# Optimization experiments

Measured on AMD Instinct MI355X. Metric: run time of the kernel, lower is better.

## Reference

```python
import jax, jax.numpy as jnp
import numpy as np

EPS = 1e-12  # torch F.normalize eps


def setup_inputs() -> dict:
    key = jax.random.key(0)
    k1, k2, k3 = jax.random.split(key, 3)
    B, D, H, W, K = 64, 512, 32, 32, 64
    x = jax.random.normal(k1, (B, D, H, W), dtype=jnp.float32)
    w = jax.random.normal(k2, (K, D), dtype=jnp.float32) * 0.05  # 1x1 conv weight
    c = jax.random.normal(k3, (K, D), dtype=jnp.float32)          # cluster centers
    return {"x": x, "w": w, "c": c}


def reference(x, w, c):
    B, D, H, W = x.shape
    K = w.shape[0]
    N = H * W
    # 1x1 conv (no bias): (B,D,H,W) x (K,D) -> (B,K,H,W)
    features = jnp.einsum('bdhw,kd->bkhw', x, w)
    # NOTE: original applies softmax over dim=2 (the H axis only)
    a_bar = jax.nn.softmax(features, axis=2)
    xf = x.reshape(B, D, N)
    a = a_bar.reshape(B, K, N)
    # V[b,k,d] = sum_n a[b,k,n] * (x[b,d,n] - c[k,d])
    V = jnp.einsum('bkn,bdn->bkd', a, xf) - a.sum(axis=2)[:, :, None] * c[None]
    V = V.transpose(2, 1, 0)  # (D, K, B)
    # F.normalize(V, p=2, dim=1) applied twice (second is idempotent)
    norm = jnp.maximum(jnp.linalg.norm(V, axis=1, keepdims=True), EPS)
    y = V / norm
    norm2 = jnp.maximum(jnp.linalg.norm(y, axis=1, keepdims=True), EPS)
    return y / norm2
```

## Files before the change

kernel.cpp:

```cpp
#include <hip/hip_runtime.h>


typedef __attribute__((ext_vector_type(8))) short short8;
typedef __attribute__((ext_vector_type(4))) float f32x4;
typedef unsigned short u16;
typedef unsigned int u32;

union S8u { u32 q[4]; short8 s; };

__device__ __forceinline__ u32 pk2(float lo, float hi) {
  union { float f; u32 u; } a, b; a.f = lo; b.f = hi;
  u32 xl = (a.u + 0x7fffu + ((a.u >> 16) & 1u)) >> 16;
  u32 xh = (b.u + 0x7fffu + ((b.u >> 16) & 1u)) & 0xffff0000u;
  return xl | xh;
}

__device__ __forceinline__ u16 bf1(float f) {
  union { float f; u32 u; } a; a.f = f;
  return (u16)((a.u + 0x7fffu + ((a.u >> 16) & 1u)) >> 16);
}

typedef const __attribute__((address_space(1))) u32 GU32;
typedef __attribute__((address_space(3))) u32 LU32;
__device__ __forceinline__ void glds16(const void* g, void* l) {
  __builtin_amdgcn_global_load_lds((GU32*)g, (LU32*)l, 16, 0, 0);
}

__global__ __launch_bounds__(256, 2) void k1_features(
    const float* __restrict__ x, const float* __restrict__ wgt,
    float* __restrict__ feat)
{
  const int blk = blockIdx.x;
  const int b = blk & 63, nt8 = blk >> 6;
  const int nb = nt8 * 128;
  const int tid = threadIdx.x, lane = tid & 63, wv = tid >> 6;
  const int row = lane & 15, q = lane >> 4;

  __shared__ __align__(16) float xs[2][32][128];

  const char* xbase = (const char*)(x + ((size_t)b << 19) + nb);
  const int dd0 = tid >> 5, cby = (tid & 31) * 16;
  const float* wrow = wgt + row * 512 + q * 8;

  f32x4 acc[4][2];
#pragma unroll
  for (int mt = 0; mt < 4; mt++)
#pragma unroll
    for (int nt = 0; nt < 2; nt++) acc[mt][nt] = (f32x4){0.f, 0.f, 0.f, 0.f};

#define STAGE1(d0, buf)                                                        \
  {                                                                            \
    char* lx = (char*)&xs[buf][0][0];                                          \
    _Pragma("unroll")                                                          \
    for (int j = 0; j < 4; j++)                                                \
      glds16(xbase + (size_t)((d0) + j * 8 + dd0) * 4096 + cby,                \
             lx + j * 4096 + tid * 16);                                        \
  }

  STAGE1(0, 0);
  f32x4 wa[4][2];
#pragma unroll
  for (int mt = 0; mt < 4; mt++) {
    wa[mt][0] = *(const f32x4*)(wrow + mt * 8192);
    wa[mt][1] = *(const f32x4*)(wrow + mt * 8192 + 4);
  }

  for (int i = 0; i < 16; i++) {
    const int buf = i & 1;
    __syncthreads();
    short8 af[4];
#pragma unroll
    for (int mt = 0; mt < 4; mt++) {
      S8u t;
      t.q[0] = pk2(wa[mt][0][0], wa[mt][0][1]); t.q[1] = pk2(wa[mt][0][2], wa[mt][0][3]);
      t.q[2] = pk2(wa[mt][1][0], wa[mt][1][1]); t.q[3] = pk2(wa[mt][1][2], wa[mt][1][3]);
      af[mt] = t.s;
    }
    if (i < 15) {
      STAGE1((i + 1) * 32, buf ^ 1);
      const float* wn = wrow + (i + 1) * 32;
#pragma unroll
      for (int mt = 0; mt < 4; mt++) {
        wa[mt][0] = *(const f32x4*)(wn + mt * 8192);
        wa[mt][1] = *(const f32x4*)(wn + mt * 8192 + 4);
      }
    }
    short8 bfv[2];
#pragma unroll
    for (int nt = 0; nt < 2; nt++) {
      const int n = wv * 32 + nt * 16 + row;
      const int d8 = q * 8;
      float v0 = xs[buf][d8 + 0][n], v1 = xs[buf][d8 + 1][n];
      float v2 = xs[buf][d8 + 2][n], v3 = xs[buf][d8 + 3][n];
      float v4 = xs[buf][d8 + 4][n], v5 = xs[buf][d8 + 5][n];
      float v6 = xs[buf][d8 + 6][n], v7 = xs[buf][d8 + 7][n];
      S8u t;
      t.q[0] = pk2(v0, v1); t.q[1] = pk2(v2, v3);
      t.q[2] = pk2(v4, v5); t.q[3] = pk2(v6, v7);
      bfv[nt] = t.s;
    }
#pragma unroll
    for (int nt = 0; nt < 2; nt++)
#pragma unroll
      for (int mt = 0; mt < 4; mt++)
        acc[mt][nt] = __builtin_amdgcn_mfma_f32_16x16x32_bf16(af[mt], bfv[nt], acc[mt][nt], 0, 0, 0);
  }
#undef STAGE1

  float* fb = feat + ((size_t)b << 16);
  const int nbw = nb + wv * 32;
#pragma unroll
  for (int mt = 0; mt < 4; mt++)
#pragma unroll
    for (int nt = 0; nt < 2; nt++)
#pragma unroll
      for (int r = 0; r < 4; r++)
        fb[(mt * 16 + q * 4 + r) * 1024 + nbw + nt * 16 + row] = acc[mt][nt][r];
}

__global__ __launch_bounds__(256) void k1b_softmax(
    const float* __restrict__ feat, u16* __restrict__ am)
{
  const int tid = threadIdx.x, lane = tid & 63, wv = tid >> 6;
  const int rid = blockIdx.x * 4 + wv;
  const float* f = feat + ((size_t)rid << 10);
  u16* ar = am + ((size_t)rid << 10);
  const int w = lane & 31, half = lane >> 5;
  const int base = w + half * 512;
  float v[16];
  float m = -1e30f;
#pragma unroll
  for (int i = 0; i < 16; i++) { v[i] = f[base + i * 32]; m = fmaxf(m, v[i]); }
  m = fmaxf(m, __shfl_xor(m, 32));
  float s = 0.f;
#pragma unroll
  for (int i = 0; i < 16; i++) { v[i] = __expf(v[i] - m); s += v[i]; }
  s += __shfl_xor(s, 32);
  const float inv = 1.0f / s;
#pragma unroll
  for (int i = 0; i < 16; i++) ar[base + i * 32] = bf1(v[i] * inv);
}

__global__ __launch_bounds__(256, 2) void k2_aggregate(
    const float* __restrict__ x, const u16* __restrict__ am,
    const float* __restrict__ cc, float* __restrict__ yw)
{
  const int blk = blockIdx.x;
  const int b = blk & 63, dt = blk >> 6;
  const int tid = threadIdx.x, lane = tid & 63, wv = tid >> 6;
  const int row = lane & 15, q = lane >> 4;

  __shared__ __align__(16) float xs[2][2048];

  const char* xbase = (const char*)(x + ((size_t)b << 19) + (size_t)dt * 64 * 1024);
  const u16* ab = am + ((size_t)b << 16) + row * 1024 + q * 8;
  const int r0 = tid >> 3, s0g = tid & 7;

#define STAGE2(n0, buf)                                                        \
  {                                                                            \
    char* lxs = (char*)&xs[buf][0];                                            \
    _Pragma("unroll")                                                          \
    for (int j = 0; j < 2; j++) {                                              \
      const int r = j * 32 + r0;                                               \
      const int col = ((s0g * 4) + ((r & 3) << 3)) & 31;                       \
      glds16(xbase + (size_t)r * 4096 + (size_t)((n0) + col) * 4,              \
             lxs + (j * 256 + tid) * 16);                                      \
    }                                                                          \
  }

  f32x4 acc[4];
#pragma unroll
  for (int mt = 0; mt < 4; mt++) acc[mt] = (f32x4){0.f, 0.f, 0.f, 0.f};

  STAGE2(0, 0);
  short8 sa[4];
#pragma unroll
  for (int mt = 0; mt < 4; mt++) sa[mt] = *(const short8*)(ab + mt * 16384);

  const int rB = wv * 16 + row;
  const int slot = (2 * q - 2 * (rB & 3)) & 7;
  const int fidx = rB * 32 + slot * 4;

  for (int i = 0; i < 32; i++) {
    const int buf = i & 1;
    __syncthreads();
    short8 af[4];
#pragma unroll
    for (int mt = 0; mt < 4; mt++) af[mt] = sa[mt];
    if (i < 31) {
      STAGE2((i + 1) * 32, buf ^ 1);
      const u16* an = ab + (i + 1) * 32;
#pragma unroll
      for (int mt = 0; mt < 4; mt++) sa[mt] = *(const short8*)(an + mt * 16384);
    }
    f32x4 g0 = *(const f32x4*)&xs[buf][fidx];
    f32x4 g1 = *(const f32x4*)&xs[buf][fidx + 4];
    S8u t;
    t.q[0] = pk2(g0[0], g0[1]); t.q[1] = pk2(g0[2], g0[3]);
    t.q[2] = pk2(g1[0], g1[1]); t.q[3] = pk2(g1[2], g1[3]);
    const short8 bfv = t.s;
#pragma unroll
    for (int mt = 0; mt < 4; mt++)
      acc[mt] = __builtin_amdgcn_mfma_f32_16x16x32_bf16(af[mt], bfv, acc[mt], 0, 0, 0);
  }
#undef STAGE2

  const int dcol = dt * 64 + wv * 16 + row;
  float v[16]; float ss = 0.f;
#pragma unroll
  for (int mt = 0; mt < 4; mt++)
#pragma unroll
    for (int r = 0; r < 4; r++) {
      const int k = mt * 16 + q * 4 + r;
      const float tv = acc[mt][r] - 32.0f * cc[k * 512 + dcol];
      v[mt * 4 + r] = tv; ss += tv * tv;
    }
  ss += __shfl_xor(ss, 16);
  ss += __shfl_xor(ss, 32);
  const float rn = 1.0f / fmaxf(sqrtf(ss), 1e-12f);
  float* yb = yw + ((size_t)b << 15) + dcol;
#pragma unroll
  for (int mt = 0; mt < 4; mt++)
#pragma unroll
    for (int r = 0; r < 4; r++)
      yb[(size_t)(mt * 16 + q * 4 + r) << 9] = v[mt * 4 + r] * rn;
}

__global__ __launch_bounds__(256) void k3_transpose(
    const float* __restrict__ yw, float* __restrict__ out)
{
  const int blk = blockIdx.x;
  const int k = blk & 63;
  const int dt = blk >> 6;
  const int d0 = dt * 64;
  const int tid = threadIdx.x;
  __shared__ float T[64][68];
  {
    const int bl = tid >> 2, seg = tid & 3;
    const float* src = yw + (size_t)bl * 32768 + k * 512 + d0 + seg * 16;
#pragma unroll
    for (int i = 0; i < 4; i++) {
      f32x4 v = *(const f32x4*)(src + i * 4);
#pragma unroll
      for (int jj = 0; jj < 4; jj++) T[seg * 16 + i * 4 + jj][bl] = v[jj];
    }
  }
  __syncthreads();
  {
    const int dl = tid >> 2, bseg = tid & 3;
    float* dst = out + (size_t)(d0 + dl) * 4096 + k * 64 + bseg * 16;
    const float* srcT = &T[dl][bseg * 16];
#pragma unroll
    for (int i = 0; i < 4; i++)
      *(f32x4*)(dst + i * 4) = *(const f32x4*)(srcT + i * 4);
  }
}

extern "C" void kernel_launch(void* const* d_in, const int* in_sizes, int n_in,
                              void* d_out, int out_size, void* d_ws, size_t ws_size,
                              hipStream_t stream) {
  const float* x = (const float*)d_in[0];
  const float* w = (const float*)d_in[1];
  const float* c = (const float*)d_in[2];
  float* out = (float*)d_out;
  char* ws = (char*)d_ws;
  float* feat = (float*)ws;
  u16*   a_ws = (u16*)(ws + (size_t)17 * 1024 * 1024);
  float* yw   = (float*)(ws + (size_t)26 * 1024 * 1024);
  k1_features <<<dim3(512),  dim3(256), 0, stream>>>(x, w, feat);
  k1b_softmax <<<dim3(1024), dim3(256), 0, stream>>>(feat, a_ws);
  k2_aggregate<<<dim3(512),  dim3(256), 0, stream>>>(x, a_ws, c, yw);
  k3_transpose<<<dim3(512),  dim3(256), 0, stream>>>(yw, out);
}
```

Before: 237.9 us.

## Fuse conv and H-axis softmax by tiling over W columns; reswizzle LDS

The conv kernel now tiles each block over 4 W columns across all 32 H rows, so the full softmax axis sits inside one block. The softmax is computed in shared memory and bf16 weights are written directly, which drops the fp32 feature round-trip through global memory and one kernel launch. The global-to-LDS load patterns in both the conv and aggregate kernels are reswizzled (rotation and XOR) to cut LDS bank conflicts. In exchange, global loads become 16-byte strided gathers of W quads, the softmax stores are scattered u16 writes, and the larger LDS footprint may limit occupancy.

```diff
diff --git a/kernel.cpp b/kernel.cpp
--- a/kernel.cpp
+++ b/kernel.cpp
@@ -26,20 +26,36 @@
   __builtin_amdgcn_global_load_lds((GU32*)g, (LU32*)l, 16, 0, 0);
 }
 
-__global__ __launch_bounds__(256, 2) void k1_features(
+__global__ __launch_bounds__(256, 2) void k1_conv_softmax(
     const float* __restrict__ x, const float* __restrict__ wgt,
-    float* __restrict__ feat)
+    u16* __restrict__ am)
 {
   const int blk = blockIdx.x;
-  const int b = blk & 63, nt8 = blk >> 6;
-  const int nb = nt8 * 128;
+  const int b = blk & 63, wq = blk >> 6;
+  const int w0 = wq * 4;
   const int tid = threadIdx.x, lane = tid & 63, wv = tid >> 6;
   const int row = lane & 15, q = lane >> 4;
 
-  __shared__ __align__(16) float xs[2][32][128];
-
-  const char* xbase = (const char*)(x + ((size_t)b << 19) + nb);
-  const int dd0 = tid >> 5, cby = (tid & 31) * 16;
+  __shared__ __align__(16) char smem[33792];
+  float (*F)[132] = (float (*)[132])smem;
+
+  int goff[4];
+#pragma unroll
+  for (int j2 = 0; j2 < 4; j2++) {
+    const int g = j2 * 256 + tid;
+    const int d = g >> 5, s = g & 31;
+    const int h = (s - 2 * (d >> 3)) & 31;
+    goff[j2] = d * 4096 + h * 128;
+  }
+  const char* xbase = (const char*)x + ((size_t)b << 21) + (size_t)w0 * 4;
+
+  int fbase[2];
+#pragma unroll
+  for (int nt = 0; nt < 2; nt++) {
+    const int j = wv * 32 + nt * 16 + row;
+    const int h = j >> 2, wl = j & 3;
+    fbase[nt] = q * 4096 + ((h + 2 * q) & 31) * 16 + wl * 4;
+  }
   const float* wrow = wgt + row * 512 + q * 8;
 
   f32x4 acc[4][2];
@@ -50,11 +66,11 @@
 
 #define STAGE1(d0, buf)                                                        \
   {                                                                            \
-    char* lx = (char*)&xs[buf][0][0];                                          \
+    char* lx = smem + (buf) * 16384;                                           \
     _Pragma("unroll")                                                          \
-    for (int j = 0; j < 4; j++)                                                \
-      glds16(xbase + (size_t)((d0) + j * 8 + dd0) * 4096 + cby,                \
-             lx + j * 4096 + tid * 16);                                        \
+    for (int j2 = 0; j2 < 4; j2++)                                             \
+      glds16(xbase + (size_t)(d0) * 4096 + goff[j2],                           \
+             lx + (j2 * 256 + tid) * 16);                                      \
   }
 
   STAGE1(0, 0);
@@ -88,12 +104,15 @@
     short8 bfv[2];
 #pragma unroll
     for (int nt = 0; nt < 2; nt++) {
-      const int n = wv * 32 + nt * 16 + row;
-      const int d8 = q * 8;
-      float v0 = xs[buf][d8 + 0][n], v1 = xs[buf][d8 + 1][n];
-      float v2 = xs[buf][d8 + 2][n], v3 = xs[buf][d8 + 3][n];
-      float v4 = xs[buf][d8 + 4][n], v5 = xs[buf][d8 + 5][n];
-      float v6 = xs[buf][d8 + 6][n], v7 = xs[buf][d8 + 7][n];
+      const char* p = smem + buf * 16384 + fbase[nt];
+      float v0 = *(const float*)(p);
+      float v1 = *(const float*)(p + 512);
+      float v2 = *(const float*)(p + 1024);
+      float v3 = *(const float*)(p + 1536);
+      float v4 = *(const float*)(p + 2048);
+      float v5 = *(const float*)(p + 2560);
+      float v6 = *(const float*)(p + 3072);
+      float v7 = *(const float*)(p + 3584);
       S8u t;
       t.q[0] = pk2(v0, v1); t.q[1] = pk2(v2, v3);
       t.q[2] = pk2(v4, v5); t.q[3] = pk2(v6, v7);
@@ -107,38 +126,34 @@
   }
 #undef STAGE1
 
-  float* fb = feat + ((size_t)b << 16);
-  const int nbw = nb + wv * 32;
+  __syncthreads();
 #pragma unroll
   for (int mt = 0; mt < 4; mt++)
 #pragma unroll
     for (int nt = 0; nt < 2; nt++)
 #pragma unroll
       for (int r = 0; r < 4; r++)
-        fb[(mt * 16 + q * 4 + r) * 1024 + nbw + nt * 16 + row] = acc[mt][nt][r];
-}
-
-__global__ __launch_bounds__(256) void k1b_softmax(
-    const float* __restrict__ feat, u16* __restrict__ am)
-{
-  const int tid = threadIdx.x, lane = tid & 63, wv = tid >> 6;
-  const int rid = blockIdx.x * 4 + wv;
-  const float* f = feat + ((size_t)rid << 10);
-  u16* ar = am + ((size_t)rid << 10);
-  const int w = lane & 31, half = lane >> 5;
-  const int base = w + half * 512;
-  float v[16];
-  float m = -1e30f;
-#pragma unroll
-  for (int i = 0; i < 16; i++) { v[i] = f[base + i * 32]; m = fmaxf(m, v[i]); }
-  m = fmaxf(m, __shfl_xor(m, 32));
-  float s = 0.f;
-#pragma unroll
-  for (int i = 0; i < 16; i++) { v[i] = __expf(v[i] - m); s += v[i]; }
-  s += __shfl_xor(s, 32);
-  const float inv = 1.0f / s;
-#pragma unroll
-  for (int i = 0; i < 16; i++) ar[base + i * 32] = bf1(v[i] * inv);
+        F[mt * 16 + q * 4 + r][wv * 32 + nt * 16 + row] = acc[mt][nt][r];
+  __syncthreads();
+
+  {
+    const int k = tid >> 2, wl = tid & 3;
+    float m = -1e30f;
+#pragma unroll
+    for (int h = 0; h < 32; h++) m = fmaxf(m, F[k][h * 4 + wl]);
+    float s = 0.f;
+#pragma unroll
+    for (int h = 0; h < 32; h++) {
+      const float e = __expf(F[k][h * 4 + wl] - m);
+      F[k][h * 4 + wl] = e;
+      s += e;
+    }
+    const float inv = 1.0f / s;
+    u16* ar = am + ((size_t)b << 16) + k * 1024 + w0 + wl;
+#pragma unroll
+    for (int h = 0; h < 32; h++)
+      ar[h * 32] = bf1(F[k][h * 4 + wl] * inv);
+  }
 }
 
 __global__ __launch_bounds__(256, 2) void k2_aggregate(
@@ -150,22 +165,30 @@
   const int tid = threadIdx.x, lane = tid & 63, wv = tid >> 6;
   const int row = lane & 15, q = lane >> 4;
 
-  __shared__ __align__(16) float xs[2][2048];
-
-  const char* xbase = (const char*)(x + ((size_t)b << 19) + (size_t)dt * 64 * 1024);
+  __shared__ __align__(16) char smem[16384];
+
+  int aoff[2];
+#pragma unroll
+  for (int j = 0; j < 2; j++) {
+    const int f = j * 256 + tid;
+    const int r = f >> 3, s = f & 7;
+    aoff[j] = r * 4096 + 4 * (s ^ (r & 7)) * 4;
+  }
+  const char* xbase = (const char*)x + ((size_t)b << 21) + (size_t)dt * 64 * 4096;
   const u16* ab = am + ((size_t)b << 16) + row * 1024 + q * 8;
-  const int r0 = tid >> 3, s0g = tid & 7;
+
+  const int rB = wv * 16 + row;
+  const int su = (2 * q) ^ (rB & 7);
+  const int fo0 = (rB * 8 + su) * 16;
+  const int fo1 = (rB * 8 + (su ^ 1)) * 16;
 
 #define STAGE2(n0, buf)                                                        \
   {                                                                            \
-    char* lxs = (char*)&xs[buf][0];                                            \
+    char* lx = smem + (buf) * 8192;                                            \
     _Pragma("unroll")                                                          \
-    for (int j = 0; j < 2; j++) {                                              \
-      const int r = j * 32 + r0;                                               \
-      const int col = ((s0g * 4) + ((r & 3) << 3)) & 31;                       \
-      glds16(xbase + (size_t)r * 4096 + (size_t)((n0) + col) * 4,              \
-             lxs + (j * 256 + tid) * 16);                                      \
-    }                                                                          \
+    for (int j = 0; j < 2; j++)                                                \
+      glds16(xbase + (size_t)(n0) * 4 + aoff[j],                               \
+             lx + (j * 256 + tid) * 16);                                       \
   }
 
   f32x4 acc[4];
@@ -176,10 +199,6 @@
   short8 sa[4];
 #pragma unroll
   for (int mt = 0; mt < 4; mt++) sa[mt] = *(const short8*)(ab + mt * 16384);
-
-  const int rB = wv * 16 + row;
-  const int slot = (2 * q - 2 * (rB & 3)) & 7;
-  const int fidx = rB * 32 + slot * 4;
 
   for (int i = 0; i < 32; i++) {
     const int buf = i & 1;
@@ -193,8 +212,8 @@
 #pragma unroll
       for (int mt = 0; mt < 4; mt++) sa[mt] = *(const short8*)(an + mt * 16384);
     }
-    f32x4 g0 = *(const f32x4*)&xs[buf][fidx];
-    f32x4 g1 = *(const f32x4*)&xs[buf][fidx + 4];
+    f32x4 g0 = *(const f32x4*)(smem + buf * 8192 + fo0);
+    f32x4 g1 = *(const f32x4*)(smem + buf * 8192 + fo1);
     S8u t;
     t.q[0] = pk2(g0[0], g0[1]); t.q[1] = pk2(g0[2], g0[3]);
     t.q[2] = pk2(g1[0], g1[1]); t.q[3] = pk2(g1[2], g1[3]);
@@ -264,11 +283,9 @@
   const float* c = (const float*)d_in[2];
   float* out = (float*)d_out;
   char* ws = (char*)d_ws;
-  float* feat = (float*)ws;
-  u16*   a_ws = (u16*)(ws + (size_t)17 * 1024 * 1024);
-  float* yw   = (float*)(ws + (size_t)26 * 1024 * 1024);
-  k1_features <<<dim3(512),  dim3(256), 0, stream>>>(x, w, feat);
-  k1b_softmax <<<dim3(1024), dim3(256), 0, stream>>>(feat, a_ws);
-  k2_aggregate<<<dim3(512),  dim3(256), 0, stream>>>(x, a_ws, c, yw);
-  k3_transpose<<<dim3(512),  dim3(256), 0, stream>>>(yw, out);
-}
+  u16*   a_ws = (u16*)ws;
+  float* yw   = (float*)(ws + (size_t)16 * 1024 * 1024);
+  k1_conv_softmax<<<dim3(512), dim3(256), 0, stream>>>(x, w, a_ws);
+  k2_aggregate   <<<dim3(512), dim3(256), 0, stream>>>(x, a_ws, c, yw);
+  k3_transpose   <<<dim3(512), dim3(256), 0, stream>>>(yw, out);
+}
```

Result: slower. 280.4 us (+17.9%).

## Pre-pack weights to bf16, stage via LDS, and XOR-swizzle aggregate x tiles

Applied to the files above, without the earlier changes.

Adds a small kernel that converts the 1x1 conv weights to padded bf16 tiles once per call. The features kernel then streams those tiles into LDS with async global-to-LDS loads instead of each thread loading fp32 weights and packing them every iteration. The aggregate kernel swaps its LDS staging pattern for an XOR swizzle to cut bank conflicts, and the softmax grid is remapped so blocks cover rows in batch-major order. The cost is one extra kernel launch and a little more shared memory in the features kernel.

```diff
diff --git a/kernel.cpp b/kernel.cpp
--- a/kernel.cpp
+++ b/kernel.cpp
@@ -2,6 +2,7 @@
 
 
 typedef __attribute__((ext_vector_type(8))) short short8;
+typedef __attribute__((ext_vector_type(8))) unsigned short u16x8;
 typedef __attribute__((ext_vector_type(4))) float f32x4;
 typedef unsigned short u16;
 typedef unsigned int u32;
@@ -26,8 +27,19 @@
   __builtin_amdgcn_global_load_lds((GU32*)g, (LU32*)l, 16, 0, 0);
 }
 
+__global__ __launch_bounds__(256) void k0_packw(
+    const float* __restrict__ w, u16* __restrict__ wsw)
+{
+  const int tg = blockIdx.x * 256 + threadIdx.x;
+  const int dd4 = tg & 7, i = (tg >> 3) & 15, k = tg >> 7;
+  f32x4 v = *(const f32x4*)(w + k * 512 + i * 32 + dd4 * 4);
+  u32* dst = (u32*)(wsw + ((size_t)i * 64 + k) * 40 + dd4 * 4);
+  dst[0] = pk2(v[0], v[1]);
+  dst[1] = pk2(v[2], v[3]);
+}
+
 __global__ __launch_bounds__(256, 2) void k1_features(
-    const float* __restrict__ x, const float* __restrict__ wgt,
+    const float* __restrict__ x, const u16* __restrict__ wsw,
     float* __restrict__ feat)
 {
   const int blk = blockIdx.x;
@@ -37,10 +49,11 @@
   const int row = lane & 15, q = lane >> 4;
 
   __shared__ __align__(16) float xs[2][32][128];
+  __shared__ __align__(16) u16 wls[2][64][40];
 
   const char* xbase = (const char*)(x + ((size_t)b << 19) + nb);
+  const char* wbase = (const char*)wsw;
   const int dd0 = tid >> 5, cby = (tid & 31) * 16;
-  const float* wrow = wgt + row * 512 + q * 8;
 
   f32x4 acc[4][2];
 #pragma unroll
@@ -52,39 +65,27 @@
   {                                                                            \
     char* lx = (char*)&xs[buf][0][0];                                          \
     _Pragma("unroll")                                                          \
-    for (int j = 0; j < 4; j++)                                                \
-      glds16(xbase + (size_t)((d0) + j * 8 + dd0) * 4096 + cby,                \
+    for (int j = 0; j < 4; j++) {                                              \
+      const int dd = j * 8 + dd0;                                              \
+      glds16(xbase + (size_t)((d0) + dd) * 4096 + cby,                         \
              lx + j * 4096 + tid * 16);                                        \
+    }                                                                          \
+    char* lw = (char*)&wls[buf][0][0];                                         \
+    const char* gw = wbase + (size_t)((d0) >> 5) * 5120;                       \
+    glds16(gw + tid * 16, lw + tid * 16);                                      \
+    if (tid < 64) glds16(gw + 4096 + tid * 16, lw + 4096 + tid * 16);          \
   }
 
   STAGE1(0, 0);
-  f32x4 wa[4][2];
-#pragma unroll
-  for (int mt = 0; mt < 4; mt++) {
-    wa[mt][0] = *(const f32x4*)(wrow + mt * 8192);
-    wa[mt][1] = *(const f32x4*)(wrow + mt * 8192 + 4);
-  }
-
   for (int i = 0; i < 16; i++) {
     const int buf = i & 1;
     __syncthreads();
+    if (i < 15) STAGE1((i + 1) * 32, buf ^ 1);
+
     short8 af[4];
 #pragma unroll
-    for (int mt = 0; mt < 4; mt++) {
-      S8u t;
-      t.q[0] = pk2(wa[mt][0][0], wa[mt][0][1]); t.q[1] = pk2(wa[mt][0][2], wa[mt][0][3]);
-      t.q[2] = pk2(wa[mt][1][0], wa[mt][1][1]); t.q[3] = pk2(wa[mt][1][2], wa[mt][1][3]);
-      af[mt] = t.s;
-    }
-    if (i < 15) {
-      STAGE1((i + 1) * 32, buf ^ 1);
-      const float* wn = wrow + (i + 1) * 32;
-#pragma unroll
-      for (int mt = 0; mt < 4; mt++) {
-        wa[mt][0] = *(const f32x4*)(wn + mt * 8192);
-        wa[mt][1] = *(const f32x4*)(wn + mt * 8192 + 4);
-      }
-    }
+    for (int mt = 0; mt < 4; mt++)
+      af[mt] = *(const short8*)&wls[buf][mt * 16 + row][q * 8];
     short8 bfv[2];
 #pragma unroll
     for (int nt = 0; nt < 2; nt++) {
@@ -121,8 +122,10 @@
 __global__ __launch_bounds__(256) void k1b_softmax(
     const float* __restrict__ feat, u16* __restrict__ am)
 {
+  const int blk = blockIdx.x;
+  const int b = blk & 63, chunk = blk >> 6;
   const int tid = threadIdx.x, lane = tid & 63, wv = tid >> 6;
-  const int rid = blockIdx.x * 4 + wv;
+  const int rid = b * 64 + chunk * 4 + wv;
   const float* f = feat + ((size_t)rid << 10);
   u16* ar = am + ((size_t)rid << 10);
   const int w = lane & 31, half = lane >> 5;
@@ -150,22 +153,30 @@
   const int tid = threadIdx.x, lane = tid & 63, wv = tid >> 6;
   const int row = lane & 15, q = lane >> 4;
 
-  __shared__ __align__(16) float xs[2][2048];
-
-  const char* xbase = (const char*)(x + ((size_t)b << 19) + (size_t)dt * 64 * 1024);
+  __shared__ __align__(16) char smem[16384];
+
+  int aoff[2];
+#pragma unroll
+  for (int j = 0; j < 2; j++) {
+    const int f = j * 256 + tid;
+    const int r = f >> 3, s = f & 7;
+    aoff[j] = r * 4096 + 4 * (s ^ (r & 7)) * 4;
+  }
+  const char* xbase = (const char*)x + ((size_t)b << 21) + (size_t)dt * 64 * 4096;
   const u16* ab = am + ((size_t)b << 16) + row * 1024 + q * 8;
-  const int r0 = tid >> 3, s0g = tid & 7;
+
+  const int rB = wv * 16 + row;
+  const int su = (2 * q) ^ (rB & 7);
+  const int fo0 = (rB * 8 + su) * 16;
+  const int fo1 = (rB * 8 + (su ^ 1)) * 16;
 
 #define STAGE2(n0, buf)                                                        \
   {                                                                            \
-    char* lxs = (char*)&xs[buf][0];                                            \
+    char* lx = smem + (buf) * 8192;                                            \
     _Pragma("unroll")                                                          \
-    for (int j = 0; j < 2; j++) {                                              \
-      const int r = j * 32 + r0;                                               \
-      const int col = ((s0g * 4) + ((r & 3) << 3)) & 31;                       \
-      glds16(xbase + (size_t)r * 4096 + (size_t)((n0) + col) * 4,              \
-             lxs + (j * 256 + tid) * 16);                                      \
-    }                                                                          \
+    for (int j = 0; j < 2; j++)                                                \
+      glds16(xbase + (size_t)(n0) * 4 + aoff[j],                               \
+             lx + (j * 256 + tid) * 16);                                       \
   }
 
   f32x4 acc[4];
@@ -176,10 +187,6 @@
   short8 sa[4];
 #pragma unroll
   for (int mt = 0; mt < 4; mt++) sa[mt] = *(const short8*)(ab + mt * 16384);
-
-  const int rB = wv * 16 + row;
-  const int slot = (2 * q - 2 * (rB & 3)) & 7;
-  const int fidx = rB * 32 + slot * 4;
 
   for (int i = 0; i < 32; i++) {
     const int buf = i & 1;
@@ -193,8 +200,8 @@
 #pragma unroll
       for (int mt = 0; mt < 4; mt++) sa[mt] = *(const short8*)(an + mt * 16384);
     }
-    f32x4 g0 = *(const f32x4*)&xs[buf][fidx];
-    f32x4 g1 = *(const f32x4*)&xs[buf][fidx + 4];
+    f32x4 g0 = *(const f32x4*)(smem + buf * 8192 + fo0);
+    f32x4 g1 = *(const f32x4*)(smem + buf * 8192 + fo1);
     S8u t;
     t.q[0] = pk2(g0[0], g0[1]); t.q[1] = pk2(g0[2], g0[3]);
     t.q[2] = pk2(g1[0], g1[1]); t.q[3] = pk2(g1[2], g1[3]);
@@ -267,7 +274,9 @@
   float* feat = (float*)ws;
   u16*   a_ws = (u16*)(ws + (size_t)17 * 1024 * 1024);
   float* yw   = (float*)(ws + (size_t)26 * 1024 * 1024);
-  k1_features <<<dim3(512),  dim3(256), 0, stream>>>(x, w, feat);
+  u16*   wsw  = (u16*)(ws + (size_t)35 * 1024 * 1024);
+  k0_packw    <<<dim3(32),   dim3(256), 0, stream>>>(w, wsw);
+  k1_features <<<dim3(512),  dim3(256), 0, stream>>>(x, wsw, feat);
   k1b_softmax <<<dim3(1024), dim3(256), 0, stream>>>(feat, a_ws);
   k2_aggregate<<<dim3(512),  dim3(256), 0, stream>>>(x, a_ws, c, yw);
   k3_transpose<<<dim3(512),  dim3(256), 0, stream>>>(yw, out);
```

Measured after the change: 241.2 us. Within noise of the previous version (+1.4%).
